# Performance work log

Hardware: AMD Instinct MI355X
Metric: run time of the kernel (lower is better)

## Reference

```python
import jax, jax.numpy as jnp
import numpy as np

N_HEAD = 4
HIDDEN = 1024
D_HEAD = HIDDEN // N_HEAD  # 256
SEQ = 1024
BATCH = 16
NEG_INF = -1e9


def setup_inputs() -> dict:
    key = jax.random.key(0)
    k1, k2, k3 = jax.random.split(key, 3)
    x = jax.random.normal(k1, (BATCH, SEQ, HIDDEN), dtype=jnp.float32)
    # torch Linear(hidden, (2n+1)*d_head, bias=False); stored here as [in, out]
    w_qkv = jax.random.normal(k2, (HIDDEN, (2 * N_HEAD + 1) * D_HEAD), dtype=jnp.float32) * (HIDDEN ** -0.5)
    # out_proj: Linear(d_head, hidden, bias=False), stored as [d_head, hidden]
    w_out = jax.random.normal(k3, (D_HEAD, HIDDEN), dtype=jnp.float32) * (D_HEAD ** -0.5)
    return {"x": x, "w_qkv": w_qkv, "w_out": w_out}


def reference(x, w_qkv, w_out):
    bs, t, h = x.shape
    n_head, d_head = N_HEAD, D_HEAD
    scale = d_head ** -0.5
    qkv = x @ w_qkv  # [bs, t, (2n+1)*d]
    q = qkv[..., : n_head * d_head].reshape(bs, t, n_head, d_head)
    k = qkv[..., n_head * d_head : 2 * n_head * d_head].reshape(bs, t, n_head, d_head)
    v = qkv[..., 2 * n_head * d_head :]  # [bs, t, d] -- single shared V
    # scores [bs, n_head, t, s]
    scores = jnp.einsum("btnd,bsnd->bnts", q, k) * scale
    causal = jnp.triu(jnp.ones((t, t), dtype=bool), 1)  # True above diag
    scores = jnp.where(causal, NEG_INF, scores)
    attn_prob = jax.nn.softmax(scores, axis=-1)  # [bs, n_head, t, s]
    attn_vec = jnp.einsum("bnts,bsd->bntd", attn_prob, v)
    m_attn_vec = jnp.mean(attn_vec, axis=1)  # mean over heads -> [bs, t, d]
    out = m_attn_vec @ w_out  # [bs, t, hidden]
    return out, attn_prob
```

## Files before the change

kernel.cpp:

```cpp
#include <hip/hip_runtime.h>
#include <hip/hip_bf16.h>
#include <type_traits>

#define BATCH  16
#define SEQ    1024
#define HIDDEN 1024
#define NHEAD  4
#define DHEAD  256
#define QKVN   2304

typedef _Float16 f16x8 __attribute__((ext_vector_type(8)));
typedef float    f32x4 __attribute__((ext_vector_type(4)));

__device__ __forceinline__ void gll16(const void* g, void* l) {
  __builtin_amdgcn_global_load_lds(
      (const __attribute__((address_space(1))) unsigned int*)g,
      (__attribute__((address_space(3))) unsigned int*)l, 16, 0, 0);
}

__global__ __launch_bounds__(256) void f32_to_f16(
    const float* __restrict__ in, _Float16* __restrict__ out) {
  int i4 = blockIdx.x * 256 + threadIdx.x;
  float4 v = ((const float4*)in)[i4];
  _Float16 h4[4] = {(_Float16)v.x, (_Float16)v.y, (_Float16)v.z, (_Float16)v.w};
  *(uint2*)&out[(size_t)i4 * 4] = *(uint2*)h4;
}

__global__ __launch_bounds__(256) void transpose_to_f16(
    const float* __restrict__ in, _Float16* __restrict__ out, int R, int C) {
  __shared__ float tile[64][65];
  int bc = blockIdx.x * 64, br = blockIdx.y * 64;
  int t = threadIdx.x;
  int tr = t >> 6, tc = t & 63;
  for (int i = 0; i < 64; i += 4)
    tile[tr + i][tc] = in[(size_t)(br + tr + i) * C + bc + tc];
  __syncthreads();
  for (int i = 0; i < 64; i += 4)
    out[(size_t)(bc + tr + i) * R + br + tc] = (_Float16)tile[tc][tr + i];
}

__device__ __forceinline__ void stage_chunk(
    const _Float16* __restrict__ G, int ldg, int k0, int rowbase,
    _Float16* ldsbase, int chunk, int t) {
  int o16 = chunk * 512 + t;
  int row = o16 >> 3;
  int c = (o16 & 7) ^ (row & 7);
  gll16(&G[(size_t)(rowbase + row) * ldg + k0 + c * 8],
        (char*)ldsbase + (size_t)o16 * 16);
}

__device__ __forceinline__ f16x8 ldsrd(const _Float16* base, int R, int ech) {
  int byte = R * 128 + ((ech * 16) ^ ((R & 7) << 4));
  return *(const f16x8*)((const char*)base + byte);
}

template <typename OT, bool FUSEV>
__global__ __launch_bounds__(512, 2) void gemm256(
    const _Float16* __restrict__ A, const _Float16* __restrict__ B,
    OT* __restrict__ C, _Float16* __restrict__ vT, int M, int N, int K) {
  __shared__ __align__(16) _Float16 lds[2][2][256][64];
  int nbm = M >> 8, nbn = N >> 8;
  int nwg = nbm * nbn;
  int lin = blockIdx.x;
  int q = nwg >> 3, r = nwg & 7;
  int xcd = lin & 7, orig = lin >> 3;
  int swz = (xcd < r ? xcd * (q + 1) : r * (q + 1) + (xcd - r) * q) + orig;
  int bm = (swz % nbm) * 256, bn = (swz / nbm) * 256;
  (void)nbn;
  int t = threadIdx.x;
  int w = t >> 6, lane = t & 63, lane15 = lane & 15, quad = lane >> 4;
  int wm = w >> 2, wn = w & 3;
  f32x4 acc[8][4] = {};
  int NT = K >> 6;
#pragma unroll
  for (int c = 0; c < 4; c++) {
    stage_chunk(A, K, 0, bm, &lds[0][0][0][0], c, t);
    stage_chunk(B, K, 0, bn, &lds[0][1][0][0], c, t);
  }
  asm volatile("s_waitcnt vmcnt(0)" ::: "memory");
  __builtin_amdgcn_s_barrier();
  __builtin_amdgcn_sched_barrier(0);
  for (int kt = 0; kt < NT; kt++) {
    int cur = kt & 1, nxt = cur ^ 1;
    int k1 = (kt + 1) << 6;
    bool prefetch = (kt + 1 < NT);
#pragma unroll
    for (int ph = 0; ph < 4; ph++) {
      int mh = ph >> 1, nh = ph & 1;
      f16x8 af[2][4], bf[2][2];
#pragma unroll
      for (int ks = 0; ks < 2; ks++) {
#pragma unroll
        for (int i = 0; i < 4; i++)
          af[ks][i] = ldsrd(&lds[cur][0][0][0],
                            wm * 128 + (mh * 4 + i) * 16 + lane15, ks * 4 + quad);
#pragma unroll
        for (int j = 0; j < 2; j++)
          bf[ks][j] = ldsrd(&lds[cur][1][0][0],
                            wn * 64 + (nh * 2 + j) * 16 + lane15, ks * 4 + quad);
      }
      if (prefetch && ph < 2) {
#pragma unroll
        for (int c = 0; c < 2; c++) {
          stage_chunk(A, K, k1, bm, &lds[nxt][0][0][0], ph * 2 + c, t);
          stage_chunk(B, K, k1, bn, &lds[nxt][1][0][0], ph * 2 + c, t);
        }
      }
      __builtin_amdgcn_s_barrier();
      __builtin_amdgcn_s_setprio(1);
#pragma unroll
      for (int ks = 0; ks < 2; ks++)
#pragma unroll
        for (int i = 0; i < 4; i++)
#pragma unroll
          for (int j = 0; j < 2; j++)
            acc[mh * 4 + i][nh * 2 + j] = __builtin_amdgcn_mfma_f32_16x16x32_f16(
                af[ks][i], bf[ks][j], acc[mh * 4 + i][nh * 2 + j], 0, 0, 0);
      __builtin_amdgcn_s_setprio(0);
      if (ph == 3 && prefetch)
        asm volatile("s_waitcnt vmcnt(0)" ::: "memory");
      __builtin_amdgcn_s_barrier();
      __builtin_amdgcn_sched_barrier(0);
    }
  }
#pragma unroll
  for (int i = 0; i < 8; i++)
#pragma unroll
    for (int j = 0; j < 4; j++) {
      int gr = bm + wm * 128 + i * 16 + quad * 4;
      int gc = bn + wn * 64 + j * 16 + lane15;
      bool tov = false;
      if constexpr (FUSEV) tov = (gc >= 2 * NHEAD * DHEAD);
      if (tov) {
        int b = gr >> 10, s = gr & 1023, d = gc - 2 * NHEAD * DHEAD;
        _Float16 h4[4];
        for (int r2 = 0; r2 < 4; r2++) h4[r2] = (_Float16)acc[i][j][r2];
        *(uint2*)&vT[((size_t)(b * DHEAD + d)) * SEQ + s] = *(uint2*)h4;
      } else {
        for (int r2 = 0; r2 < 4; r2++) {
          float v = acc[i][j][r2];
          if constexpr (std::is_same_v<OT, float>)
            C[(size_t)(gr + r2) * N + gc] = v;
          else
            C[(size_t)(gr + r2) * N + gc] = (_Float16)v;
        }
      }
    }
}

__global__ __launch_bounds__(512, 2) void scores_norm_kernel(
    const _Float16* __restrict__ qkv, float* __restrict__ P) {
  int lin = blockIdx.x + 16 * (blockIdx.y + 4 * blockIdx.z);
  int swz = (lin & 7) * 128 + (lin >> 3);
  int ti = swz & 15, n = (swz >> 4) & 3, b = swz >> 6;
  __shared__ __align__(16) _Float16 Qs[8][64][32];
  __shared__ __align__(16) _Float16 Ks[2][8][64][32];
  int t = threadIdx.x;
  int w = t >> 6, L = t & 63, lane15 = L & 15, quad = L >> 4;
  int r16 = (w & 3) * 16;
  int ch  = (w >> 2) * 32;
  for (int r = 0; r < 4; r++) {
    int u = t + r * 512;
    int kc = u >> 8, row = (u & 255) >> 2, c8 = u & 3;
    gll16(&qkv[((size_t)(b * SEQ + ti * 64 + row)) * QKVN + n * DHEAD + kc * 32 + c8 * 8],
          &Qs[kc][row][c8 * 8]);
    gll16(&qkv[((size_t)(b * SEQ + row)) * QKVN + NHEAD * DHEAD + n * DHEAD + kc * 32 + c8 * 8],
          &Ks[0][kc][row][c8 * 8]);
  }
  __syncthreads();
  f16x8 aq[8];
#pragma unroll
  for (int kc = 0; kc < 8; kc++) aq[kc] = *(f16x8*)&Qs[kc][r16 + lane15][quad * 8];
  f32x4 s[16][2];
  int trow = ti * 64 + r16 + quad * 4;
  const float scale = 0.0625f;
#pragma unroll
  for (int si = 0; si < 16; si++) {
    if (si <= ti) {
      if (si < ti) {
        for (int r = 0; r < 4; r++) {
          int u = t + r * 512;
          int kc = u >> 8, row = (u & 255) >> 2, c8 = u & 3;
          gll16(&qkv[((size_t)(b * SEQ + (si + 1) * 64 + row)) * QKVN + NHEAD * DHEAD + n * DHEAD + kc * 32 + c8 * 8],
                &Ks[(si + 1) & 1][kc][row][c8 * 8]);
        }
      }
      s[si][0] = (f32x4){0.f, 0.f, 0.f, 0.f};
      s[si][1] = (f32x4){0.f, 0.f, 0.f, 0.f};
      for (int kc = 0; kc < 8; kc++) {
        for (int j = 0; j < 2; j++) {
          f16x8 bk = *(f16x8*)&Ks[si & 1][kc][ch + j * 16 + lane15][quad * 8];
          s[si][j] = __builtin_amdgcn_mfma_f32_16x16x32_f16(aq[kc], bk, s[si][j], 0, 0, 0);
        }
      }
      __syncthreads();
    }
  }
  float m[4], l[4];
#pragma unroll
  for (int r = 0; r < 4; r++) {
    float mx = -INFINITY;
#pragma unroll
    for (int si = 0; si < 16; si++) {
      if (si <= ti) {
        for (int j = 0; j < 2; j++) {
          int col = si * 64 + ch + j * 16 + lane15;
          float v = s[si][j][r] * scale;
          if (col > trow + r) v = -1e9f;
          s[si][j][r] = v;
          mx = fmaxf(mx, v);
        }
      }
    }
    for (int off = 1; off < 16; off <<= 1) mx = fmaxf(mx, __shfl_xor(mx, off, 64));
    float sum = 0.f;
#pragma unroll
    for (int si = 0; si < 16; si++) {
      if (si <= ti) {
        for (int j = 0; j < 2; j++) {
          float p = __expf(s[si][j][r] - mx);
          s[si][j][r] = p;
          sum += p;
        }
      }
    }
    for (int off = 1; off < 16; off <<= 1) sum += __shfl_xor(sum, off, 64);
    m[r] = mx; l[r] = sum;
  }
  __syncthreads();
  float* sM  = (float*)&Qs[0][0][0];
  float* sL  = sM + 128;
  float* sMc = sM + 256;
  float* sRl = sM + 320;
  if (lane15 == 0) {
    for (int r = 0; r < 4; r++) {
      sM[(w >> 2) * 64 + r16 + quad * 4 + r] = m[r];
      sL[(w >> 2) * 64 + r16 + quad * 4 + r] = l[r];
    }
  }
  __syncthreads();
  if (t < 64) {
    float m0 = sM[t], m1 = sM[64 + t], l0 = sL[t], l1 = sL[64 + t];
    float mc = fmaxf(m0, m1);
    float lc = l0 * __expf(m0 - mc) + l1 * __expf(m1 - mc);
    sMc[t] = mc;
    sRl[t] = 1.0f / lc;
  }
  __syncthreads();
  float fac[4];
  for (int r = 0; r < 4; r++) {
    int row = r16 + quad * 4 + r;
    fac[r] = __expf(m[r] - sMc[row]) * sRl[row];
  }
  size_t Pbase = ((size_t)(b * NHEAD + n)) * SEQ * SEQ;
#pragma unroll
  for (int si = 0; si < 16; si++) {
    if (si <= ti) {
      for (int j = 0; j < 2; j++) {
        int col = si * 64 + ch + j * 16 + lane15;
        for (int r = 0; r < 4; r++)
          P[Pbase + (size_t)(trow + r) * SEQ + col] = s[si][j][r] * fac[r];
      }
    }
  }
  {
    float4 z = make_float4(0.f, 0.f, 0.f, 0.f);
    int c4min = (ti + 1) * 16;
    for (int u = t; u < 16384; u += 512) {
      int row = u >> 8, c4 = u & 255;
      if (c4 >= c4min)
        *(float4*)&P[Pbase + (size_t)(ti * 64 + row) * SEQ + c4 * 4] = z;
    }
  }
}

__global__ __launch_bounds__(256) void pmean_kernel(
    const float* __restrict__ P, _Float16* __restrict__ Pmean) {
  int si = blockIdx.x, ti = blockIdx.y, b = blockIdx.z;
  if (si > ti) return;
  int t = threadIdx.x;
  int row = t >> 2, c16 = (t & 3) * 16;
  size_t tile_off = (size_t)(ti * 64 + row) * SEQ + si * 64 + c16;
  float acc[16];
  for (int i = 0; i < 16; i++) acc[i] = 0.f;
  for (int n = 0; n < 4; n++) {
    const float* p = &P[((size_t)(b * NHEAD + n)) * SEQ * SEQ + tile_off];
    for (int q = 0; q < 4; q++) {
      float4 v = *(const float4*)(p + q * 4);
      acc[q * 4 + 0] += v.x; acc[q * 4 + 1] += v.y;
      acc[q * 4 + 2] += v.z; acc[q * 4 + 3] += v.w;
    }
  }
  _Float16 h[16];
  for (int i = 0; i < 16; i++) h[i] = (_Float16)(acc[i] * 0.25f);
  _Float16* pm = &Pmean[((size_t)(b * SEQ + ti * 64 + row)) * SEQ + si * 64 + c16];
  *(uint4*)pm = *(uint4*)h;
  *(uint4*)(pm + 8) = *(uint4*)(h + 8);
}

__global__ __launch_bounds__(256) void pv_kernel(
    const _Float16* __restrict__ Pmean, const _Float16* __restrict__ vT,
    _Float16* __restrict__ mattn) {
  int lin = blockIdx.x + 16 * (blockIdx.y + 4 * blockIdx.z);
  int swz = (lin & 7) * 128 + (lin >> 3);
  int ti = swz & 15, dq = (swz >> 4) & 3, b = swz >> 6;
  __shared__ __align__(16) _Float16 Pm[2][2][64][32];
  __shared__ __align__(16) _Float16 Vs[2][2][64][32];
  int t = threadIdx.x;
  int w = t >> 6, L = t & 63, lane15 = L & 15, quad = L >> 4;
  f32x4 acc[4] = {};
  for (int r = 0; r < 2; r++) {
    int u = t + r * 256;
    int kc = u >> 8, row = (u & 255) >> 2, c8 = u & 3;
    gll16(&Pmean[((size_t)(b * SEQ + ti * 64 + row)) * SEQ + kc * 32 + c8 * 8],
          &Pm[0][kc][row][c8 * 8]);
    gll16(&vT[((size_t)(b * DHEAD + dq * 64 + row)) * SEQ + kc * 32 + c8 * 8],
          &Vs[0][kc][row][c8 * 8]);
  }
  __syncthreads();
  for (int si = 0; si <= ti; si++) {
    int cb = si & 1;
    if (si < ti) {
      for (int r = 0; r < 2; r++) {
        int u = t + r * 256;
        int kc = u >> 8, row = (u & 255) >> 2, c8 = u & 3;
        gll16(&Pmean[((size_t)(b * SEQ + ti * 64 + row)) * SEQ + (si + 1) * 64 + kc * 32 + c8 * 8],
              &Pm[cb ^ 1][kc][row][c8 * 8]);
        gll16(&vT[((size_t)(b * DHEAD + dq * 64 + row)) * SEQ + (si + 1) * 64 + kc * 32 + c8 * 8],
              &Vs[cb ^ 1][kc][row][c8 * 8]);
      }
    }
#pragma unroll
    for (int kc = 0; kc < 2; kc++) {
      f16x8 ap = *(f16x8*)&Pm[cb][kc][w * 16 + lane15][quad * 8];
#pragma unroll
      for (int j = 0; j < 4; j++) {
        f16x8 bv = *(f16x8*)&Vs[cb][kc][j * 16 + lane15][quad * 8];
        acc[j] = __builtin_amdgcn_mfma_f32_16x16x32_f16(ap, bv, acc[j], 0, 0, 0);
      }
    }
    __syncthreads();
  }
  for (int j = 0; j < 4; j++) {
    int row = b * SEQ + ti * 64 + w * 16 + quad * 4;
    int col = dq * 64 + j * 16 + lane15;
    for (int r = 0; r < 4; r++)
      mattn[(size_t)(row + r) * DHEAD + col] = (_Float16)acc[j][r];
  }
}

extern "C" void kernel_launch(void* const* d_in, const int* in_sizes, int n_in,
                              void* d_out, int out_size, void* d_ws, size_t ws_size,
                              hipStream_t stream) {
  const float* x     = (const float*)d_in[0];
  const float* w_qkv = (const float*)d_in[1];
  const float* w_out = (const float*)d_in[2];
  float* out = (float*)d_out;
  float* P   = out + (size_t)BATCH * SEQ * HIDDEN;

  _Float16* wqkvT = (_Float16*)d_ws;
  _Float16* woutT = wqkvT + (size_t)QKVN * HIDDEN;
  _Float16* qkvb  = woutT + (size_t)HIDDEN * DHEAD;
  _Float16* vT    = qkvb + (size_t)BATCH * SEQ * QKVN;
  _Float16* mattn = qkvb;
  _Float16* Pmean = qkvb + (size_t)BATCH * SEQ * DHEAD;
  _Float16* xh    = (_Float16*)P;

  f32_to_f16<<<BATCH * SEQ * HIDDEN / 1024, 256, 0, stream>>>(x, xh);
  transpose_to_f16<<<dim3(QKVN / 64, HIDDEN / 64), 256, 0, stream>>>(w_qkv, wqkvT, HIDDEN, QKVN);
  transpose_to_f16<<<dim3(HIDDEN / 64, DHEAD / 64), 256, 0, stream>>>(w_out, woutT, DHEAD, HIDDEN);
  gemm256<_Float16, true><<<(BATCH * SEQ / 256) * (QKVN / 256), 512, 0, stream>>>(
      xh, wqkvT, qkvb, vT, BATCH * SEQ, QKVN, HIDDEN);
  scores_norm_kernel<<<dim3(SEQ / 64, NHEAD, BATCH), 512, 0, stream>>>(qkvb, P);
  pmean_kernel<<<dim3(SEQ / 64, SEQ / 64, BATCH), 256, 0, stream>>>(P, Pmean);
  pv_kernel<<<dim3(SEQ / 64, 4, BATCH), 256, 0, stream>>>(Pmean, vT, mattn);
  gemm256<float, false><<<(BATCH * SEQ / 256) * (HIDDEN / 256), 512, 0, stream>>>(
      mattn, woutT, out, nullptr, BATCH * SEQ, HIDDEN, DHEAD);
}
```

Measured before the change: 642.7 us.

## Fuse prep kernels, triple-buffer K loads in scores kernel, compact pmean grid

Three prep launches (x to f16 and two weight transposes) are merged into one kernel that picks its job from the block index. The scores kernel now loads Q straight into registers instead of staging it in LDS, and keeps three K buffers with explicit vmcnt waits, raw barriers and s_setprio so K loads overlap the MFMA work. pmean launches only the lower-triangle tiles, recovering (ti, si) with a sqrt-based index, so no blocks exit immediately. The risks are heavier register use, hand-counted vmcnt thresholds that must match the number of loads in flight, and the cost of the sqrt index recovery.

```diff
diff --git a/kernel.cpp b/kernel.cpp
--- a/kernel.cpp
+++ b/kernel.cpp
@@ -18,19 +18,31 @@
       (__attribute__((address_space(3))) unsigned int*)l, 16, 0, 0);
 }
 
-__global__ __launch_bounds__(256) void f32_to_f16(
-    const float* __restrict__ in, _Float16* __restrict__ out) {
-  int i4 = blockIdx.x * 256 + threadIdx.x;
-  float4 v = ((const float4*)in)[i4];
-  _Float16 h4[4] = {(_Float16)v.x, (_Float16)v.y, (_Float16)v.z, (_Float16)v.w};
-  *(uint2*)&out[(size_t)i4 * 4] = *(uint2*)h4;
-}
-
-__global__ __launch_bounds__(256) void transpose_to_f16(
-    const float* __restrict__ in, _Float16* __restrict__ out, int R, int C) {
+__global__ __launch_bounds__(256) void prep_kernel(
+    const float* __restrict__ x, _Float16* __restrict__ xh,
+    const float* __restrict__ w_qkv, _Float16* __restrict__ wqkvT,
+    const float* __restrict__ w_out, _Float16* __restrict__ woutT) {
   __shared__ float tile[64][65];
-  int bc = blockIdx.x * 64, br = blockIdx.y * 64;
+  int bid = blockIdx.x;
   int t = threadIdx.x;
+  if (bid < 16384) {
+    int i4 = bid * 256 + t;
+    float4 v = ((const float4*)x)[i4];
+    _Float16 h4[4] = {(_Float16)v.x, (_Float16)v.y, (_Float16)v.z, (_Float16)v.w};
+    *(uint2*)&xh[(size_t)i4 * 4] = *(uint2*)h4;
+    return;
+  }
+  const float* in; _Float16* out; int R, C, bx, by;
+  if (bid < 16384 + 576) {
+    int u = bid - 16384;
+    in = w_qkv; out = wqkvT; R = HIDDEN; C = QKVN;
+    bx = u % 36; by = u / 36;
+  } else {
+    int u = bid - 16960;
+    in = w_out; out = woutT; R = DHEAD; C = HIDDEN;
+    bx = u % 16; by = u / 16;
+  }
+  int bc = bx * 64, br = by * 64;
   int tr = t >> 6, tc = t & 63;
   for (int i = 0; i < 64; i += 4)
     tile[tr + i][tc] = in[(size_t)(br + tr + i) * C + bc + tc];
@@ -153,49 +165,61 @@
   int lin = blockIdx.x + 16 * (blockIdx.y + 4 * blockIdx.z);
   int swz = (lin & 7) * 128 + (lin >> 3);
   int ti = swz & 15, n = (swz >> 4) & 3, b = swz >> 6;
-  __shared__ __align__(16) _Float16 Qs[8][64][32];
-  __shared__ __align__(16) _Float16 Ks[2][8][64][32];
+  __shared__ __align__(16) _Float16 Ks[3][8][64][32];
+  __shared__ float scratch[384];
   int t = threadIdx.x;
   int w = t >> 6, L = t & 63, lane15 = L & 15, quad = L >> 4;
   int r16 = (w & 3) * 16;
   int ch  = (w >> 2) * 32;
-  for (int r = 0; r < 4; r++) {
-    int u = t + r * 512;
-    int kc = u >> 8, row = (u & 255) >> 2, c8 = u & 3;
-    gll16(&qkv[((size_t)(b * SEQ + ti * 64 + row)) * QKVN + n * DHEAD + kc * 32 + c8 * 8],
-          &Qs[kc][row][c8 * 8]);
-    gll16(&qkv[((size_t)(b * SEQ + row)) * QKVN + NHEAD * DHEAD + n * DHEAD + kc * 32 + c8 * 8],
-          &Ks[0][kc][row][c8 * 8]);
-  }
-  __syncthreads();
   f16x8 aq[8];
 #pragma unroll
-  for (int kc = 0; kc < 8; kc++) aq[kc] = *(f16x8*)&Qs[kc][r16 + lane15][quad * 8];
+  for (int kc = 0; kc < 8; kc++)
+    aq[kc] = *(const f16x8*)&qkv[((size_t)(b * SEQ + ti * 64 + r16 + lane15)) * QKVN
+                                 + n * DHEAD + kc * 32 + quad * 8];
+  asm volatile("s_waitcnt vmcnt(0)" ::: "memory");
+
+#define STAGEK(si_, buf_)                                                     \
+  for (int r_ = 0; r_ < 4; r_++) {                                            \
+    int u_ = t + r_ * 512;                                                    \
+    int kc_ = u_ >> 8, row_ = (u_ & 255) >> 2, c8_ = u_ & 3;                  \
+    gll16(&qkv[((size_t)(b * SEQ + (si_) * 64 + row_)) * QKVN                 \
+               + NHEAD * DHEAD + n * DHEAD + kc_ * 32 + c8_ * 8],             \
+          &Ks[buf_][kc_][row_][c8_ * 8]);                                     \
+  }
+
+  STAGEK(0, 0);
+  if (ti >= 1) STAGEK(1, 1);
+
   f32x4 s[16][2];
   int trow = ti * 64 + r16 + quad * 4;
   const float scale = 0.0625f;
 #pragma unroll
   for (int si = 0; si < 16; si++) {
     if (si <= ti) {
-      if (si < ti) {
-        for (int r = 0; r < 4; r++) {
-          int u = t + r * 512;
-          int kc = u >> 8, row = (u & 255) >> 2, c8 = u & 3;
-          gll16(&qkv[((size_t)(b * SEQ + (si + 1) * 64 + row)) * QKVN + NHEAD * DHEAD + n * DHEAD + kc * 32 + c8 * 8],
-                &Ks[(si + 1) & 1][kc][row][c8 * 8]);
-        }
-      }
+      if (si + 2 <= ti) { STAGEK(si + 2, (si + 2) % 3); }
+      int d = ti - si;
+      if (d >= 2)      asm volatile("s_waitcnt vmcnt(8)" ::: "memory");
+      else if (d == 1) asm volatile("s_waitcnt vmcnt(4)" ::: "memory");
+      else             asm volatile("s_waitcnt vmcnt(0)" ::: "memory");
+      __builtin_amdgcn_s_barrier();
+      __builtin_amdgcn_sched_barrier(0);
       s[si][0] = (f32x4){0.f, 0.f, 0.f, 0.f};
       s[si][1] = (f32x4){0.f, 0.f, 0.f, 0.f};
+      __builtin_amdgcn_s_setprio(1);
+#pragma unroll
       for (int kc = 0; kc < 8; kc++) {
+#pragma unroll
         for (int j = 0; j < 2; j++) {
-          f16x8 bk = *(f16x8*)&Ks[si & 1][kc][ch + j * 16 + lane15][quad * 8];
+          f16x8 bk = *(f16x8*)&Ks[si % 3][kc][ch + j * 16 + lane15][quad * 8];
           s[si][j] = __builtin_amdgcn_mfma_f32_16x16x32_f16(aq[kc], bk, s[si][j], 0, 0, 0);
         }
       }
-      __syncthreads();
-    }
-  }
+      __builtin_amdgcn_s_setprio(0);
+      __builtin_amdgcn_s_barrier();
+      __builtin_amdgcn_sched_barrier(0);
+    }
+  }
+#undef STAGEK
   float m[4], l[4];
 #pragma unroll
   for (int r = 0; r < 4; r++) {
@@ -228,10 +252,10 @@
     m[r] = mx; l[r] = sum;
   }
   __syncthreads();
-  float* sM  = (float*)&Qs[0][0][0];
-  float* sL  = sM + 128;
-  float* sMc = sM + 256;
-  float* sRl = sM + 320;
+  float* sM  = scratch;
+  float* sL  = scratch + 128;
+  float* sMc = scratch + 256;
+  float* sRl = scratch + 320;
   if (lane15 == 0) {
     for (int r = 0; r < 4; r++) {
       sM[(w >> 2) * 64 + r16 + quad * 4 + r] = m[r];
@@ -276,8 +300,11 @@
 
 __global__ __launch_bounds__(256) void pmean_kernel(
     const float* __restrict__ P, _Float16* __restrict__ Pmean) {
-  int si = blockIdx.x, ti = blockIdx.y, b = blockIdx.z;
-  if (si > ti) return;
+  int u = blockIdx.x, b = blockIdx.y;
+  int ti = (int)((__fsqrt_rn(8.f * u + 1.f) - 1.f) * 0.5f);
+  while ((ti + 1) * (ti + 2) / 2 <= u) ++ti;
+  while (ti * (ti + 1) / 2 > u) --ti;
+  int si = u - ti * (ti + 1) / 2;
   int t = threadIdx.x;
   int row = t >> 2, c16 = (t & 3) * 16;
   size_t tile_off = (size_t)(ti * 64 + row) * SEQ + si * 64 + c16;
@@ -366,13 +393,11 @@
   _Float16* Pmean = qkvb + (size_t)BATCH * SEQ * DHEAD;
   _Float16* xh    = (_Float16*)P;
 
-  f32_to_f16<<<BATCH * SEQ * HIDDEN / 1024, 256, 0, stream>>>(x, xh);
-  transpose_to_f16<<<dim3(QKVN / 64, HIDDEN / 64), 256, 0, stream>>>(w_qkv, wqkvT, HIDDEN, QKVN);
-  transpose_to_f16<<<dim3(HIDDEN / 64, DHEAD / 64), 256, 0, stream>>>(w_out, woutT, DHEAD, HIDDEN);
+  prep_kernel<<<16384 + 576 + 64, 256, 0, stream>>>(x, xh, w_qkv, wqkvT, w_out, woutT);
   gemm256<_Float16, true><<<(BATCH * SEQ / 256) * (QKVN / 256), 512, 0, stream>>>(
       xh, wqkvT, qkvb, vT, BATCH * SEQ, QKVN, HIDDEN);
   scores_norm_kernel<<<dim3(SEQ / 64, NHEAD, BATCH), 512, 0, stream>>>(qkvb, P);
-  pmean_kernel<<<dim3(SEQ / 64, SEQ / 64, BATCH), 256, 0, stream>>>(P, Pmean);
+  pmean_kernel<<<dim3(136, BATCH), 256, 0, stream>>>(P, Pmean);
   pv_kernel<<<dim3(SEQ / 64, 4, BATCH), 256, 0, stream>>>(Pmean, vT, mattn);
   gemm256<float, false><<<(BATCH * SEQ / 256) * (HIDDEN / 256), 512, 0, stream>>>(
       mattn, woutT, out, nullptr, BATCH * SEQ, HIDDEN, DHEAD);
```

Result: no change. 634.7 us (-1.2%).
